# Kernel optimization log

Hardware: AMD Instinct MI355X
Metric: run time of the kernel (lower is better)

The kernel has to match this reference:

```python
import jax, jax.numpy as jnp
import numpy as np

B, N, E = 4, 10000, 80000
DN, DE, DG = 64, 16, 32
D, H, L = 256, 8, 3
DH = D // H


def _ln(x, s, b, eps=1e-6):
    m = x.mean(-1, keepdims=True)
    v = ((x - m) ** 2).mean(-1, keepdims=True)
    return (x - m) * jax.lax.rsqrt(v + eps) * s + b


def setup_inputs() -> dict:
    key = jax.random.key(0)
    ks = jax.random.split(key, 20)
    sc = 0.02
    p = {}
    # graph data
    p['node_features'] = jax.random.normal(ks[0], (B, N, DN), jnp.float32)
    p['edge_features'] = jax.random.normal(ks[1], (B, E, DE), jnp.float32)
    p['global_features'] = jax.random.normal(ks[2], (B, 1, DG), jnp.float32)
    p['edge_list'] = jax.random.randint(ks[3], (B, E, 2), 0, N)
    p['edge_mask'] = jax.random.bernoulli(ks[4], 0.9, (B, E))
    p['node_mask'] = jax.random.bernoulli(ks[5], 0.95, (B, N))
    p['current_agent_node_ind'] = jax.random.randint(ks[6], (B,), 0, N)
    # input projections
    p['W_node_in'] = jax.random.normal(ks[7], (DN + DG, D)) * sc
    p['b_node_in'] = jnp.zeros((D,))
    p['W_edge_in'] = jax.random.normal(ks[8], (DE, D)) * sc
    p['b_edge_in'] = jnp.zeros((D,))
    p['ln_edge_s'] = jnp.ones((D,)); p['ln_edge_b'] = jnp.zeros((D,))
    # stacked GCN layers: message Dense over concat([h_sender, edge_feat])
    p['gcn_W'] = jax.random.normal(ks[9], (L, 2 * D, D)) * sc
    p['gcn_b'] = jnp.zeros((L, D))
    p['ln_s'] = jnp.ones((L, D)); p['ln_b'] = jnp.zeros((L, D))
    # PGAT params
    p['lnq_s'] = jnp.ones((D,)); p['lnq_b'] = jnp.zeros((D,))
    p['lnk_s'] = jnp.ones((D,)); p['lnk_b'] = jnp.zeros((D,))
    p['Wq'] = jax.random.normal(ks[10], (D, D)) * sc; p['bq'] = jnp.zeros((D,))
    p['Wk'] = jax.random.normal(ks[11], (D, D)) * sc; p['bk'] = jnp.zeros((D,))
    p['Wv'] = jax.random.normal(ks[12], (D, D)) * sc; p['bv'] = jnp.zeros((D,))
    p['Wo'] = jax.random.normal(ks[13], (D, D)) * sc; p['bo'] = jnp.zeros((D,))
    p['lnf_s'] = jnp.ones((D,)); p['lnf_b'] = jnp.zeros((D,))
    return p


def reference(node_features, edge_features, global_features, edge_list, edge_mask,
              node_mask, current_agent_node_ind,
              W_node_in, b_node_in, W_edge_in, b_edge_in, ln_edge_s, ln_edge_b,
              gcn_W, gcn_b, ln_s, ln_b,
              lnq_s, lnq_b, lnk_s, lnk_b, Wq, bq, Wk, bk, Wv, bv, Wo, bo,
              lnf_s, lnf_b):
    senders = edge_list[..., 0]
    receivers = edge_list[..., 1]
    # masked-edge handling: original sets indices to -1 so scatter drops them;
    # we mask explicitly (same math) with safe indices.
    s_safe = jnp.where(edge_mask, senders, 0)
    r_safe = jnp.where(edge_mask, receivers, 0)
    emf = edge_mask.astype(node_features.dtype)  # [B, E]

    gf = jnp.broadcast_to(global_features, node_features.shape[:-1] + (DG,))
    h = jnp.concatenate([node_features, gf], axis=-1) @ W_node_in + b_node_in  # [B,N,D]
    e = jax.nn.relu(_ln(edge_features @ W_edge_in + b_edge_in, ln_edge_s, ln_edge_b))  # [B,E,D]

    seg = jax.vmap(lambda m, r: jax.ops.segment_sum(m, r, num_segments=N))
    deg = jnp.maximum(seg(emf[..., None], r_safe), 1.0)  # [B,N,1]

    for i in range(L):
        hn = jax.nn.relu(_ln(h, ln_s[i], ln_b[i]))
        hs = jnp.take_along_axis(hn, s_safe[..., None], axis=-2)  # [B,E,D] gather
        msg = jnp.concatenate([hs, e], axis=-1) @ gcn_W[i] + gcn_b[i]
        msg = msg * emf[..., None]
        agg = seg(msg, r_safe) / deg  # normalized (mean) aggregation
        h = hn + agg  # residual

    # agent node gather: [B,1,D]
    q_in = jnp.take_along_axis(h, current_agent_node_ind[:, None, None], axis=-2)

    # PGAT: masked multi-head attention of agent query over all nodes
    q = _ln(q_in, lnq_s, lnq_b)
    k = _ln(h, lnk_s, lnk_b)
    Q = (q @ Wq + bq).reshape(B, 1, H, DH)
    K = (k @ Wk + bk).reshape(B, N, H, DH)
    V = (k @ Wv + bv).reshape(B, N, H, DH)
    scores = jnp.einsum('bqhd,bkhd->bhqk', Q, K) / jnp.asarray(np.sqrt(DH), Q.dtype)
    scores = jnp.where(node_mask[:, None, None, :], scores, -1e9)
    attn = jax.nn.softmax(scores, axis=-1)
    o = jnp.einsum('bhqk,bkhd->bqhd', attn, V).reshape(B, 1, D)
    x = q_in + (o @ Wo + bo)  # residual
    x = jax.nn.relu(_ln(x, lnf_s, lnf_b))
    return x.reshape(B, D)  # rearrange '... n d -> ... (n d)' with n=1
```

## Files before the change

### kernel.cpp

```cpp
#include <hip/hip_runtime.h>
#include <hip/hip_bf16.h>

#define B_ 4
#define N_ 10000
#define E_ 80000
#define D_ 256
#define BN_ (B_*N_)
#define MPAD 40064
#define SCAN_NBLK ((BN_ + 255) / 256)

typedef __attribute__((ext_vector_type(8))) short short8;
typedef __attribute__((ext_vector_type(4))) float f32x4;
typedef __attribute__((ext_vector_type(4))) unsigned short u16x4;

static __device__ __forceinline__ float wave_sum(float v){
  #pragma unroll
  for(int o=32;o>0;o>>=1) v += __shfl_xor(v, o);
  return v;
}

static __device__ __forceinline__ float block_sum(float v, float* red){
  v = wave_sum(v);
  int w = threadIdx.x >> 6;
  if((threadIdx.x & 63) == 0) red[w] = v;
  __syncthreads();
  float r = (red[0] + red[1]) + (red[2] + red[3]);
  __syncthreads();
  return r;
}

static __device__ __forceinline__ unsigned short f2bf(float f){
  unsigned u = __float_as_uint(f);
  return (unsigned short)((u + 0x7fffu + ((u>>16)&1u)) >> 16);
}
static __device__ __forceinline__ float bf2f(unsigned short b){
  return __uint_as_float(((unsigned)b) << 16);
}

__global__ __launch_bounds__(256) void k_node_in(
    const float* __restrict__ nf, const float* __restrict__ gf,
    const float* __restrict__ W, const float* __restrict__ bias,
    const float* __restrict__ lns, const float* __restrict__ lnb,
    unsigned short* __restrict__ hnbf){
  __shared__ float in_s[16][96];
  __shared__ float h_s[16][256];
  int base = blockIdx.x * 16;
  int tid = threadIdx.x;
  for(int idx = tid; idx < 16*96; idx += 256){
    int i = idx / 96, k = idx - i*96;
    int row = base + i;
    int b = row / N_;
    float v = (k < 64) ? nf[(size_t)row*64 + k] : gf[b*32 + (k-64)];
    in_s[i][k] = v;
  }
  __syncthreads();
  int c = tid;
  float acc[16];
  #pragma unroll
  for(int i=0;i<16;i++) acc[i]=0.f;
  for(int k=0;k<96;k+=4){
    float w0 = W[(k+0)*D_+c], w1 = W[(k+1)*D_+c];
    float w2 = W[(k+2)*D_+c], w3 = W[(k+3)*D_+c];
    #pragma unroll
    for(int i=0;i<16;i++){
      float4 a = *reinterpret_cast<const float4*>(&in_s[i][k]);
      acc[i] += a.x*w0 + a.y*w1 + a.z*w2 + a.w*w3;
    }
  }
  float bc = bias[c];
  #pragma unroll
  for(int i=0;i<16;i++) h_s[i][c] = acc[i] + bc;
  __syncthreads();
  int wv = tid>>6, lane = tid&63;
  float4 s4 = *reinterpret_cast<const float4*>(&lns[lane*4]);
  float4 b4 = *reinterpret_cast<const float4*>(&lnb[lane*4]);
  #pragma unroll
  for(int rr=0; rr<4; ++rr){
    int i = wv*4 + rr;
    float4 x = *reinterpret_cast<const float4*>(&h_s[i][lane*4]);
    float sum = x.x+x.y+x.z+x.w;
    float sq = x.x*x.x+x.y*x.y+x.z*x.z+x.w*x.w;
    #pragma unroll
    for(int o=32;o>0;o>>=1){ sum += __shfl_xor(sum,o); sq += __shfl_xor(sq,o); }
    float mean = sum*(1.f/256.f);
    float var = sq*(1.f/256.f) - mean*mean;
    float rs = rsqrtf(var + 1e-6f);
    u16x4 o;
    o.x = f2bf(fmaxf((x.x-mean)*rs*s4.x + b4.x, 0.f));
    o.y = f2bf(fmaxf((x.y-mean)*rs*s4.y + b4.y, 0.f));
    o.z = f2bf(fmaxf((x.z-mean)*rs*s4.z + b4.z, 0.f));
    o.w = f2bf(fmaxf((x.w-mean)*rs*s4.w + b4.w, 0.f));
    *reinterpret_cast<u16x4*>(&hnbf[(size_t)(base+i)*D_ + lane*4]) = o;
  }
}

__global__ __launch_bounds__(256) void k_hist(
    const int* __restrict__ el, const int* __restrict__ emask,
    int* __restrict__ counts){
  int e = blockIdx.x*256 + threadIdx.x;
  if(e >= B_*E_) return;
  if(emask[e]){
    int b = e / E_;
    int r = el[(size_t)e*2 + 1];
    atomicAdd(&counts[b*N_ + r], 1);
  }
}

__global__ __launch_bounds__(256) void k_scanA(
    const int* __restrict__ counts, int* __restrict__ bsum){
  __shared__ int red[4];
  int idx = blockIdx.x*256 + threadIdx.x;
  int x = (idx < BN_) ? counts[idx] : 0;
  int lane = threadIdx.x & 63, w = threadIdx.x >> 6;
  int s = x;
  #pragma unroll
  for(int o=32;o>0;o>>=1) s += __shfl_xor(s, o);
  if(lane == 0) red[w] = s;
  __syncthreads();
  if(threadIdx.x == 0) bsum[blockIdx.x] = red[0]+red[1]+red[2]+red[3];
}

__global__ __launch_bounds__(256) void k_scanB(
    const int* __restrict__ bsum, int* __restrict__ boff){
  __shared__ int ws[4];
  int t = threadIdx.x;
  int x = (t < SCAN_NBLK) ? bsum[t] : 0;
  int lane = t & 63, w = t >> 6;
  int incl = x;
  #pragma unroll
  for(int o=1;o<64;o<<=1){ int v=__shfl_up(incl,o); if(lane>=o) incl+=v; }
  if(lane == 63) ws[w] = incl;
  __syncthreads();
  int pre = 0;
  for(int i=0;i<w;i++) pre += ws[i];
  if(t < SCAN_NBLK) boff[t] = pre + incl - x;
}

__global__ __launch_bounds__(256) void k_scanC(
    const int* __restrict__ counts, const int* __restrict__ boff,
    int* __restrict__ offsets){
  __shared__ int ws[4];
  int idx = blockIdx.x*256 + threadIdx.x;
  int x = (idx < BN_) ? counts[idx] : 0;
  int lane = threadIdx.x & 63, w = threadIdx.x >> 6;
  int incl = x;
  #pragma unroll
  for(int o=1;o<64;o<<=1){ int v=__shfl_up(incl,o); if(lane>=o) incl+=v; }
  if(lane == 63) ws[w] = incl;
  __syncthreads();
  int pre = boff[blockIdx.x];
  for(int i=0;i<w;i++) pre += ws[i];
  int excl = pre + incl - x;
  if(idx < BN_) offsets[idx] = excl;
  if(idx == BN_-1) offsets[BN_] = excl + x;
}

__global__ __launch_bounds__(256) void k_eprep(
    const float* __restrict__ W, const float* __restrict__ be,
    float* __restrict__ prep){
  int t = threadIdx.x;
  int i = t >> 4, j = t & 15;
  float m = 0.f;
  for(int c=0;c<256;c++) m += W[i*256+c]*W[j*256+c];
  prep[t] = m;
  if(t < 16){
    float v=0.f, wb=0.f;
    for(int c=0;c<256;c++){ v += W[t*256+c]*be[c]; wb += W[t*256+c]; }
    prep[256+t] = v;
    prep[272+t] = wb*(1.f/256.f);
  }
  if(t == 0){
    float bb=0.f, ss=0.f;
    for(int c=0;c<256;c++){ bb += be[c]; ss += be[c]*be[c]; }
    prep[288] = bb*(1.f/256.f);
    prep[289] = ss;
  }
}

__global__ __launch_bounds__(256) void k_fill(
    const int* __restrict__ el, const int* __restrict__ emask,
    const float* __restrict__ ef, const float* __restrict__ prep,
    const int* __restrict__ offsets, int* __restrict__ cursor,
    int* __restrict__ s_send, float* __restrict__ ef_slot,
    float* __restrict__ stats){
  __shared__ float M_s[290];
  for(int i=threadIdx.x; i<290; i+=256) M_s[i] = prep[i];
  __syncthreads();
  int e = blockIdx.x*256 + threadIdx.x;
  if(e >= B_*E_) return;
  if(!emask[e]) return;
  int b = e / E_;
  int s = el[(size_t)e*2], r = el[(size_t)e*2 + 1];
  int bn = b*N_ + r;
  int pos = offsets[bn] + atomicAdd(&cursor[bn], 1);
  s_send[pos] = b*N_ + s;
  const float4* src = reinterpret_cast<const float4*>(ef + (size_t)e*16);
  float4 f0=src[0], f1=src[1], f2=src[2], f3=src[3];
  float4* dst = reinterpret_cast<float4*>(ef_slot + (size_t)pos*16);
  dst[0]=f0; dst[1]=f1; dst[2]=f2; dst[3]=f3;
  float f[16] = {f0.x,f0.y,f0.z,f0.w, f1.x,f1.y,f1.z,f1.w,
                 f2.x,f2.y,f2.z,f2.w, f3.x,f3.y,f3.z,f3.w};
  float mean = M_s[288];
  #pragma unroll
  for(int k=0;k<16;k++) mean += f[k]*M_s[272+k];
  float q = M_s[289];
  #pragma unroll
  for(int i=0;i<16;i++){
    float pi = 2.f*M_s[256+i];
    #pragma unroll
    for(int j=0;j<16;j++) pi += M_s[i*16+j]*f[j];
    q += f[i]*pi;
  }
  float var = q*(1.f/256.f) - mean*mean;
  float rstd = rsqrtf(var + 1e-6f);
  stats[(size_t)pos*2]   = mean;
  stats[(size_t)pos*2+1] = rstd;
}

__global__ __launch_bounds__(256) void k_wt(
    const float* __restrict__ gcnW, unsigned short* __restrict__ Wt){
  __shared__ float sm[32][33];
  int bid = blockIdx.x;
  int l = bid >> 7;
  int t = bid & 127;
  int k0 = (t >> 3)*32, n0 = (t & 7)*32;
  int r = threadIdx.x >> 3;
  int c4 = (threadIdx.x & 7)*4;
  const float* src = gcnW + (size_t)l*512*256;
  float4 v = *reinterpret_cast<const float4*>(&src[(size_t)(k0+r)*256 + n0 + c4]);
  sm[r][c4+0]=v.x; sm[r][c4+1]=v.y; sm[r][c4+2]=v.z; sm[r][c4+3]=v.w;
  __syncthreads();
  u16x4 o;
  o.x = f2bf(sm[c4+0][r]); o.y = f2bf(sm[c4+1][r]);
  o.z = f2bf(sm[c4+2][r]); o.w = f2bf(sm[c4+3][r]);
  *reinterpret_cast<u16x4*>(&Wt[(size_t)l*256*512 + (size_t)(n0+r)*512 + k0 + c4]) = o;
}

#define PROJ(F0,F1,F2,F3,COMP) (be4.COMP \
  + F0.x*w[0].COMP + F0.y*w[1].COMP + F0.z*w[2].COMP + F0.w*w[3].COMP \
  + F1.x*w[4].COMP + F1.y*w[5].COMP + F1.z*w[6].COMP + F1.w*w[7].COMP \
  + F2.x*w[8].COMP + F2.y*w[9].COMP + F2.z*w[10].COMP + F2.w*w[11].COMP \
  + F3.x*w[12].COMP + F3.y*w[13].COMP + F3.z*w[14].COMP + F3.w*w[15].COMP)

__global__ __launch_bounds__(256) void k_se_wave(
    const float* __restrict__ ef_slot, const float* __restrict__ stats,
    const float* __restrict__ W, const float* __restrict__ be,
    const float* __restrict__ lns, const float* __restrict__ lnb,
    const int* __restrict__ offsets, unsigned short* __restrict__ Abf){
  int bn = blockIdx.x*4 + (threadIdx.x>>6);
  int lane = threadIdx.x & 63;
  int c = lane*4;
  float4 w[16];
  #pragma unroll
  for(int k=0;k<16;k++) w[k] = *reinterpret_cast<const float4*>(&W[k*D_ + c]);
  float4 be4 = *reinterpret_cast<const float4*>(&be[c]);
  float4 s4  = *reinterpret_cast<const float4*>(&lns[c]);
  float4 b4  = *reinterpret_cast<const float4*>(&lnb[c]);
  int beg = __builtin_amdgcn_readfirstlane(offsets[bn]);
  int end = __builtin_amdgcn_readfirstlane(offsets[bn+1]);
  float a0=0.f,a1=0.f,a2=0.f,a3=0.f;
  int slot = beg;
  for(; slot+2 <= end; slot += 2){
    const float4* e0 = reinterpret_cast<const float4*>(ef_slot + (size_t)slot*16);
    const float4* e1 = reinterpret_cast<const float4*>(ef_slot + (size_t)(slot+1)*16);
    float2 st0 = *reinterpret_cast<const float2*>(stats + (size_t)slot*2);
    float2 st1 = *reinterpret_cast<const float2*>(stats + (size_t)(slot+1)*2);
    float4 f0=e0[0], f1=e0[1], f2=e0[2], f3=e0[3];
    float4 g0=e1[0], g1=e1[1], g2=e1[2], g3=e1[3];
    float t0=PROJ(f0,f1,f2,f3,x), t1=PROJ(f0,f1,f2,f3,y);
    float t2=PROJ(f0,f1,f2,f3,z), t3=PROJ(f0,f1,f2,f3,w);
    float u0=PROJ(g0,g1,g2,g3,x), u1=PROJ(g0,g1,g2,g3,y);
    float u2=PROJ(g0,g1,g2,g3,z), u3=PROJ(g0,g1,g2,g3,w);
    float m0=st0.x, r0=st0.y, m1=st1.x, r1=st1.y;
    a0 += fmaxf((t0-m0)*r0*s4.x + b4.x, 0.f) + fmaxf((u0-m1)*r1*s4.x + b4.x, 0.f);
    a1 += fmaxf((t1-m0)*r0*s4.y + b4.y, 0.f) + fmaxf((u1-m1)*r1*s4.y + b4.y, 0.f);
    a2 += fmaxf((t2-m0)*r0*s4.z + b4.z, 0.f) + fmaxf((u2-m1)*r1*s4.z + b4.z, 0.f);
    a3 += fmaxf((t3-m0)*r0*s4.w + b4.w, 0.f) + fmaxf((u3-m1)*r1*s4.w + b4.w, 0.f);
  }
  if(slot < end){
    const float4* e0 = reinterpret_cast<const float4*>(ef_slot + (size_t)slot*16);
    float2 st0 = *reinterpret_cast<const float2*>(stats + (size_t)slot*2);
    float4 f0=e0[0], f1=e0[1], f2=e0[2], f3=e0[3];
    float t0=PROJ(f0,f1,f2,f3,x), t1=PROJ(f0,f1,f2,f3,y);
    float t2=PROJ(f0,f1,f2,f3,z), t3=PROJ(f0,f1,f2,f3,w);
    float m0=st0.x, r0=st0.y;
    a0 += fmaxf((t0-m0)*r0*s4.x + b4.x, 0.f);
    a1 += fmaxf((t1-m0)*r0*s4.y + b4.y, 0.f);
    a2 += fmaxf((t2-m0)*r0*s4.z + b4.z, 0.f);
    a3 += fmaxf((t3-m0)*r0*s4.w + b4.w, 0.f);
  }
  u16x4 o; o.x=f2bf(a0); o.y=f2bf(a1); o.z=f2bf(a2); o.w=f2bf(a3);
  *reinterpret_cast<u16x4*>(Abf + (size_t)bn*512 + 256 + c) = o;
}

__global__ __launch_bounds__(256) void k_ln_relu(
    const float* __restrict__ h, const float* __restrict__ s,
    const float* __restrict__ b, unsigned short* __restrict__ hnbf){
  int row = blockIdx.x*4 + (threadIdx.x>>6);
  int lane = threadIdx.x & 63;
  int c = lane*4;
  float4 x = *reinterpret_cast<const float4*>(&h[(size_t)row*D_ + c]);
  float sum = x.x+x.y+x.z+x.w;
  float sq = x.x*x.x+x.y*x.y+x.z*x.z+x.w*x.w;
  #pragma unroll
  for(int o=32;o>0;o>>=1){ sum += __shfl_xor(sum,o); sq += __shfl_xor(sq,o); }
  float mean = sum*(1.f/256.f);
  float var = sq*(1.f/256.f) - mean*mean;
  float rs = rsqrtf(var + 1e-6f);
  float4 s4 = *reinterpret_cast<const float4*>(&s[c]);
  float4 b4 = *reinterpret_cast<const float4*>(&b[c]);
  u16x4 o;
  o.x = f2bf(fmaxf((x.x-mean)*rs*s4.x + b4.x, 0.f));
  o.y = f2bf(fmaxf((x.y-mean)*rs*s4.y + b4.y, 0.f));
  o.z = f2bf(fmaxf((x.z-mean)*rs*s4.z + b4.z, 0.f));
  o.w = f2bf(fmaxf((x.w-mean)*rs*s4.w + b4.w, 0.f));
  *reinterpret_cast<u16x4*>(&hnbf[(size_t)row*D_ + c]) = o;
}

__global__ __launch_bounds__(256) void k_agg(
    const unsigned short* __restrict__ hnbf, const int* __restrict__ offsets,
    const int* __restrict__ s_send, unsigned short* __restrict__ Abf){
  int bn = blockIdx.x*4 + (threadIdx.x>>6);
  int lane = threadIdx.x & 63;
  int beg = __builtin_amdgcn_readfirstlane(offsets[bn]);
  int end = __builtin_amdgcn_readfirstlane(offsets[bn+1]);
  float a0=0.f,a1=0.f,a2=0.f,a3=0.f;
  int slot = beg;
  for(; slot+4 <= end; slot += 4){
    int sr0 = s_send[slot],   sr1 = s_send[slot+1];
    int sr2 = s_send[slot+2], sr3 = s_send[slot+3];
    u16x4 v0 = *reinterpret_cast<const u16x4*>(hnbf + (size_t)sr0*D_ + lane*4);
    u16x4 v1 = *reinterpret_cast<const u16x4*>(hnbf + (size_t)sr1*D_ + lane*4);
    u16x4 v2 = *reinterpret_cast<const u16x4*>(hnbf + (size_t)sr2*D_ + lane*4);
    u16x4 v3 = *reinterpret_cast<const u16x4*>(hnbf + (size_t)sr3*D_ + lane*4);
    a0 += bf2f(v0.x)+bf2f(v1.x)+bf2f(v2.x)+bf2f(v3.x);
    a1 += bf2f(v0.y)+bf2f(v1.y)+bf2f(v2.y)+bf2f(v3.y);
    a2 += bf2f(v0.z)+bf2f(v1.z)+bf2f(v2.z)+bf2f(v3.z);
    a3 += bf2f(v0.w)+bf2f(v1.w)+bf2f(v2.w)+bf2f(v3.w);
  }
  for(; slot < end; ++slot){
    int sr = s_send[slot];
    u16x4 v = *reinterpret_cast<const u16x4*>(hnbf + (size_t)sr*D_ + lane*4);
    a0 += bf2f(v.x); a1 += bf2f(v.y); a2 += bf2f(v.z); a3 += bf2f(v.w);
  }
  u16x4 o; o.x=f2bf(a0); o.y=f2bf(a1); o.z=f2bf(a2); o.w=f2bf(a3);
  *reinterpret_cast<u16x4*>(Abf + (size_t)bn*512 + lane*4) = o;
}

__global__ __launch_bounds__(256) void k_gemm_mfma(
    const unsigned short* __restrict__ Abf,
    const unsigned short* __restrict__ Wt,
    const float* __restrict__ bias,
    const int* __restrict__ counts,
    const unsigned short* __restrict__ hnbf,
    float* __restrict__ hout){
  __shared__ unsigned short A_s[128*32];
  __shared__ unsigned short B_s[128*32];
  int bid = blockIdx.x;
  int row0 = (bid>>1)*128;
  int col0 = (bid&1)*128;
  int tid = threadIdx.x;
  int lane = tid & 63;
  int wid = tid >> 6;
  int wr = wid >> 1, wc = wid & 1;
  f32x4 acc[4][4];
  #pragma unroll
  for(int m=0;m<4;m++)
    #pragma unroll
    for(int n=0;n<4;n++) acc[m][n] = (f32x4){0.f,0.f,0.f,0.f};

  int sr = tid >> 1;
  int sc0 = (tid & 1)*2;
  const unsigned short* agp = Abf + (size_t)(row0+sr)*512;
  const unsigned short* bgp = Wt  + (size_t)(col0+sr)*512;
  unsigned swA0 = (unsigned)(sr*64 + (((sc0  ) ^ (sr&3))*16));
  unsigned swA1 = (unsigned)(sr*64 + (((sc0+1) ^ (sr&3))*16));
  int frow = lane & 15;
  int fsw = (lane >> 4) ^ (lane & 3);

  for(int k0=0; k0<512; k0+=32){
    short8 a0 = *reinterpret_cast<const short8*>(agp + k0 + sc0*8);
    short8 a1 = *reinterpret_cast<const short8*>(agp + k0 + sc0*8 + 8);
    short8 b0 = *reinterpret_cast<const short8*>(bgp + k0 + sc0*8);
    short8 b1 = *reinterpret_cast<const short8*>(bgp + k0 + sc0*8 + 8);
    __syncthreads();
    *reinterpret_cast<short8*>((char*)A_s + swA0) = a0;
    *reinterpret_cast<short8*>((char*)A_s + swA1) = a1;
    *reinterpret_cast<short8*>((char*)B_s + swA0) = b0;
    *reinterpret_cast<short8*>((char*)B_s + swA1) = b1;
    __syncthreads();
    short8 af[4], bfr[4];
    #pragma unroll
    for(int m=0;m<4;m++){
      int r = wr*64 + m*16 + frow;
      af[m] = *reinterpret_cast<const short8*>((const char*)A_s + r*64 + fsw*16);
    }
    #pragma unroll
    for(int n=0;n<4;n++){
      int r = wc*64 + n*16 + frow;
      bfr[n] = *reinterpret_cast<const short8*>((const char*)B_s + r*64 + fsw*16);
    }
    #pragma unroll
    for(int m=0;m<4;m++)
      #pragma unroll
      for(int n=0;n<4;n++)
        acc[m][n] = __builtin_amdgcn_mfma_f32_16x16x32_bf16(af[m], bfr[n], acc[m][n], 0, 0, 0);
  }
  #pragma unroll
  for(int m=0;m<4;m++){
    #pragma unroll
    for(int n=0;n<4;n++){
      int col = col0 + wc*64 + n*16 + (lane&15);
      int rbase = row0 + wr*64 + m*16 + (lane>>4)*4;
      float bcol = bias[col];
      #pragma unroll
      for(int j=0;j<4;j++){
        int r = rbase + j;
        if(r < BN_){
          float cnt = (float)counts[r];
          float inv = 1.f / fmaxf(cnt, 1.f);
          hout[(size_t)r*D_ + col] = bf2f(hnbf[(size_t)r*D_ + col]) + (acc[m][n][j] + cnt*bcol)*inv;
        }
      }
    }
  }
}

__global__ __launch_bounds__(256) void k_qprep(
    const float* __restrict__ h, const int* __restrict__ agent,
    const float* __restrict__ lnq_s, const float* __restrict__ lnq_b,
    const float* __restrict__ Wq, const float* __restrict__ bq,
    const float* __restrict__ Wk, const float* __restrict__ bk,
    float* __restrict__ q_in, float* __restrict__ Wq_eff,
    float* __restrict__ qconst){
  __shared__ float q_s[256];
  __shared__ float Q_s[256];
  __shared__ float red[4];
  int b = blockIdx.x, c = threadIdx.x;
  size_t row = (size_t)(b*N_ + agent[b]);
  float x = h[row*D_ + c];
  q_in[b*D_ + c] = x;
  float s1 = block_sum(x, red);
  float mean = s1*(1.f/256.f);
  float d = x - mean;
  float s2 = block_sum(d*d, red);
  float q = d * rsqrtf(s2*(1.f/256.f) + 1e-6f) * lnq_s[c] + lnq_b[c];
  q_s[c] = q;
  __syncthreads();
  float acc = bq[c];
  for(int k=0;k<256;k++) acc += q_s[k]*Wq[k*D_ + c];
  Q_s[c] = acc;
  __syncthreads();
  const float scale = 0.17677669529663687f;
  for(int idx=c; idx<2048; idx+=256){
    int hh = idx >> 8, dd = idx & 255;
    const float4* wk4 = reinterpret_cast<const float4*>(&Wk[(size_t)dd*D_ + hh*32]);
    const float4* q4  = reinterpret_cast<const float4*>(&Q_s[hh*32]);
    float t = 0.f;
    #pragma unroll
    for(int k4=0;k4<8;k4++){
      float4 w = wk4[k4]; float4 qq = q4[k4];
      t += w.x*qq.x + w.y*qq.y + w.z*qq.z + w.w*qq.w;
    }
    Wq_eff[b*2048 + hh*256 + dd] = t*scale;
  }
  if(c < 8){
    float t = 0.f;
    for(int dh=0; dh<32; dh++) t += Q_s[c*32+dh]*bk[c*32+dh];
    qconst[b*8 + c] = t*scale;
  }
}

__global__ __launch_bounds__(256) void k_scores(
    const float* __restrict__ h, const float* __restrict__ lnk_s,
    const float* __restrict__ lnk_b, const float* __restrict__ Wq_eff,
    const float* __restrict__ qconst, const int* __restrict__ nmask,
    unsigned short* __restrict__ kbuf, float* __restrict__ scores){
  __shared__ float wq_s[2048];
  int row0 = blockIdx.x * 4;
  int b = row0 / N_;
  for(int i=threadIdx.x; i<2048; i+=256) wq_s[i] = Wq_eff[b*2048 + i];
  __syncthreads();
  int wave = threadIdx.x >> 6, lane = threadIdx.x & 63;
  int row = row0 + wave;
  int n = row - b*N_;
  int c = lane*4;
  float4 x = *reinterpret_cast<const float4*>(&h[(size_t)row*D_ + c]);
  float sum = x.x+x.y+x.z+x.w;
  float sq = x.x*x.x+x.y*x.y+x.z*x.z+x.w*x.w;
  #pragma unroll
  for(int o=32;o>0;o>>=1){ sum += __shfl_xor(sum,o); sq += __shfl_xor(sq,o); }
  float mean = sum*(1.f/256.f);
  float var = sq*(1.f/256.f) - mean*mean;
  float rs = rsqrtf(var + 1e-6f);
  float4 s4 = *reinterpret_cast<const float4*>(&lnk_s[c]);
  float4 b4 = *reinterpret_cast<const float4*>(&lnk_b[c]);
  float4 kv;
  kv.x = (x.x-mean)*rs*s4.x + b4.x;
  kv.y = (x.y-mean)*rs*s4.y + b4.y;
  kv.z = (x.z-mean)*rs*s4.z + b4.z;
  kv.w = (x.w-mean)*rs*s4.w + b4.w;
  u16x4 kb; kb.x=f2bf(kv.x); kb.y=f2bf(kv.y); kb.z=f2bf(kv.z); kb.w=f2bf(kv.w);
  *reinterpret_cast<u16x4*>(&kbuf[(size_t)row*D_ + c]) = kb;
  bool valid = nmask[row] != 0;
  #pragma unroll
  for(int hh=0; hh<8; hh++){
    float4 w = *reinterpret_cast<const float4*>(&wq_s[hh*256 + c]);
    float p = kv.x*w.x + kv.y*w.y + kv.z*w.z + kv.w*w.w;
    p = wave_sum(p);
    if(lane==0) scores[(size_t)(b*8+hh)*N_ + n] = valid ? (p + qconst[b*8+hh]) : -1e9f;
  }
}

__global__ __launch_bounds__(256) void k_softA(
    const float* __restrict__ scores, float* __restrict__ pm,
    float* __restrict__ ps){
  __shared__ float red[4];
  int bh = blockIdx.x / 10;
  int c0 = (blockIdx.x % 10) * 1000;
  int tid = threadIdx.x;
  float m = -3e38f;
  for(int n=tid; n<1000; n+=256) m = fmaxf(m, scores[(size_t)bh*N_ + c0 + n]);
  #pragma unroll
  for(int o=32;o>0;o>>=1) m = fmaxf(m, __shfl_xor(m,o));
  if((tid&63)==0) red[tid>>6] = m;
  __syncthreads();
  m = fmaxf(fmaxf(red[0],red[1]), fmaxf(red[2],red[3]));
  __syncthreads();
  float s = 0.f;
  for(int n=tid; n<1000; n+=256) s += __expf(scores[(size_t)bh*N_ + c0 + n] - m);
  s = block_sum(s, red);
  if(tid==0){ pm[blockIdx.x] = m; ps[blockIdx.x] = s; }
}

__global__ __launch_bounds__(64) void k_softB(
    const float* __restrict__ pm, const float* __restrict__ ps,
    float* __restrict__ mg, float* __restrict__ inv){
  int t = threadIdx.x;
  if(t < 32){
    float m = -3e38f;
    #pragma unroll
    for(int c=0;c<10;c++) m = fmaxf(m, pm[t*10+c]);
    float s = 0.f;
    #pragma unroll
    for(int c=0;c<10;c++) s += ps[t*10+c]*__expf(pm[t*10+c]-m);
    mg[t] = m;
    inv[t] = 1.f/s;
  }
}

__global__ __launch_bounds__(256) void k_kbar(
    const unsigned short* __restrict__ kbuf, const float* __restrict__ scores,
    const float* __restrict__ mg, const float* __restrict__ inv,
    float* __restrict__ kbar){
  __shared__ float p_s[8][40];
  int b = blockIdx.x / 250;
  int n0 = (blockIdx.x % 250) * 40;
  for(int i=threadIdx.x; i<8*40; i+=256){
    int hh = i/40, nn = i - hh*40;
    p_s[hh][nn] = __expf(scores[(size_t)(b*8+hh)*N_ + n0 + nn] - mg[b*8+hh]);
  }
  __syncthreads();
  int c = threadIdx.x;
  float acc[8] = {0.f,0.f,0.f,0.f,0.f,0.f,0.f,0.f};
  for(int nn=0; nn<40; ++nn){
    float kv = bf2f(kbuf[(size_t)(b*N_ + n0 + nn)*D_ + c]);
    #pragma unroll
    for(int hh=0;hh<8;hh++) acc[hh] += p_s[hh][nn]*kv;
  }
  #pragma unroll
  for(int hh=0;hh<8;hh++)
    atomicAdd(&kbar[(b*8+hh)*D_ + c], acc[hh]*inv[b*8+hh]);
}

__global__ __launch_bounds__(256) void k_final(
    const float* __restrict__ kbar, const float* __restrict__ Wv,
    const float* __restrict__ bv, const float* __restrict__ Wo,
    const float* __restrict__ bo, const float* __restrict__ q_in,
    const float* __restrict__ lnf_s, const float* __restrict__ lnf_b,
    float* __restrict__ out){
  __shared__ float kb_s[2048];
  __shared__ float o_s[256];
  __shared__ float red[4];
  int b = blockIdx.x, c = threadIdx.x;
  for(int i=c; i<2048; i+=256) kb_s[i] = kbar[b*2048 + i];
  __syncthreads();
  int hh = c >> 5;
  float o = bv[c];
  for(int d=0; d<256; d++) o += kb_s[hh*256 + d]*Wv[(size_t)d*D_ + c];
  o_s[c] = o;
  __syncthreads();
  float y = bo[c] + q_in[b*D_ + c];
  for(int d=0; d<256; d++) y += o_s[d]*Wo[(size_t)d*D_ + c];
  float s1 = block_sum(y, red);
  float mean = s1*(1.f/256.f);
  float dd = y - mean;
  float s2 = block_sum(dd*dd, red);
  float v = dd * rsqrtf(s2*(1.f/256.f) + 1e-6f) * lnf_s[c] + lnf_b[c];
  out[b*D_ + c] = fmaxf(v, 0.f);
}

extern "C" void kernel_launch(void* const* d_in, const int* in_sizes, int n_in,
                              void* d_out, int out_size, void* d_ws, size_t ws_size,
                              hipStream_t stream){
  const float* nf    = (const float*)d_in[0];
  const float* ef    = (const float*)d_in[1];
  const float* gf    = (const float*)d_in[2];
  const int*   el    = (const int*)d_in[3];
  const int*   emask = (const int*)d_in[4];
  const int*   nmask = (const int*)d_in[5];
  const int*   agent = (const int*)d_in[6];
  const float* W_node = (const float*)d_in[7];
  const float* b_node = (const float*)d_in[8];
  const float* W_edge = (const float*)d_in[9];
  const float* b_edge = (const float*)d_in[10];
  const float* ln_e_s = (const float*)d_in[11];
  const float* ln_e_b = (const float*)d_in[12];
  const float* gcn_W  = (const float*)d_in[13];
  const float* gcn_b  = (const float*)d_in[14];
  const float* ln_s   = (const float*)d_in[15];
  const float* ln_b   = (const float*)d_in[16];
  const float* lnq_s  = (const float*)d_in[17];
  const float* lnq_b  = (const float*)d_in[18];
  const float* lnk_s  = (const float*)d_in[19];
  const float* lnk_b  = (const float*)d_in[20];
  const float* Wq = (const float*)d_in[21];
  const float* bq = (const float*)d_in[22];
  const float* Wk = (const float*)d_in[23];
  const float* bk = (const float*)d_in[24];
  const float* Wv = (const float*)d_in[25];
  const float* bv = (const float*)d_in[26];
  const float* Wo = (const float*)d_in[27];
  const float* bo = (const float*)d_in[28];
  const float* lnf_s = (const float*)d_in[29];
  const float* lnf_b = (const float*)d_in[30];
  float* out = (float*)d_out;

  const size_t ND = (size_t)BN_*D_;
  char* w = (char*)d_ws;
  float* h_buf = (float*)w;                   w += ND*4;
  unsigned short* hn_bf = (unsigned short*)w; w += (size_t)MPAD*D_*2;
  unsigned short* A_bf = (unsigned short*)w;  w += (size_t)MPAD*512*2;
  unsigned short* Wt = (unsigned short*)w;    w += (size_t)3*256*512*2;
  float* scores = (float*)w;                  w += (size_t)B_*8*N_*4;
  float* q_in = (float*)w;                    w += B_*D_*4;
  float* Wq_eff = (float*)w;                  w += B_*8*D_*4;
  float* qconst = (float*)w;                  w += B_*8*4;
  float* pm = (float*)w;                      w += 320*4;
  float* ps = (float*)w;                      w += 320*4;
  float* mg = (float*)w;                      w += 32*4;
  float* invs = (float*)w;                    w += 32*4;
  float* kbar = (float*)w;                    w += B_*8*D_*4;
  float* prep = (float*)w;                    w += 512*4;
  int* counts = (int*)w;                      w += BN_*4;
  int* cursor = (int*)w;                      w += BN_*4;
  int* offsets = (int*)w;                     w += (BN_+1)*4;
  int* bsum = (int*)w;                        w += SCAN_NBLK*4;
  int* boff = (int*)w;                        w += SCAN_NBLK*4;
  int* s_send = (int*)w;                      w += (size_t)B_*E_*4;
  float* ef_slot = (float*)w;                 w += (size_t)B_*E_*16*4;
  float* stats = (float*)w;                   w += (size_t)B_*E_*2*4;
  unsigned short* kbuf = (unsigned short*)A_bf;

  hipMemsetAsync(counts, 0, sizeof(int)*(size_t)2*BN_, stream);
  hipMemsetAsync(kbar, 0, sizeof(float)*(size_t)B_*8*D_, stream);

  k_node_in<<<BN_/16, 256, 0, stream>>>(nf, gf, W_node, b_node, ln_s, ln_b, hn_bf);
  k_hist<<<B_*E_/256, 256, 0, stream>>>(el, emask, counts);
  k_scanA<<<SCAN_NBLK, 256, 0, stream>>>(counts, bsum);
  k_scanB<<<1, 256, 0, stream>>>(bsum, boff);
  k_scanC<<<SCAN_NBLK, 256, 0, stream>>>(counts, boff, offsets);
  k_eprep<<<1, 256, 0, stream>>>(W_edge, b_edge, prep);
  k_fill<<<B_*E_/256, 256, 0, stream>>>(el, emask, ef, prep, offsets, cursor,
                                        s_send, ef_slot, stats);
  k_wt<<<384, 256, 0, stream>>>(gcn_W, Wt);
  k_se_wave<<<BN_/4, 256, 0, stream>>>(ef_slot, stats, W_edge, b_edge,
                                       ln_e_s, ln_e_b, offsets, A_bf);

  for(int i=0;i<3;i++){
    k_agg<<<BN_/4, 256, 0, stream>>>(hn_bf, offsets, s_send, A_bf);
    k_gemm_mfma<<<(MPAD/128)*2, 256, 0, stream>>>(A_bf, Wt + (size_t)i*256*512,
                                                  gcn_b + i*D_, counts, hn_bf, h_buf);
    if(i < 2)
      k_ln_relu<<<BN_/4, 256, 0, stream>>>(h_buf, ln_s + (i+1)*D_, ln_b + (i+1)*D_, hn_bf);
  }

  k_qprep<<<B_, 256, 0, stream>>>(h_buf, agent, lnq_s, lnq_b, Wq, bq, Wk, bk,
                                  q_in, Wq_eff, qconst);
  k_scores<<<BN_/4, 256, 0, stream>>>(h_buf, lnk_s, lnk_b, Wq_eff, qconst, nmask,
                                      kbuf, scores);
  k_softA<<<320, 256, 0, stream>>>(scores, pm, ps);
  k_softB<<<1, 64, 0, stream>>>(pm, ps, mg, invs);
  k_kbar<<<B_*250, 256, 0, stream>>>(kbuf, scores, mg, invs, kbar);
  k_final<<<B_, 256, 0, stream>>>(kbar, Wv, bv, Wo, bo, q_in, lnf_s, lnf_b, out);
}
```

Measured before the change: 481.1 us.

## Fuse layer-norm and ReLU into GCN GEMM epilogue with full-row tiles

The GEMM now computes full 256-column rows per block, using 512 threads and a 128x256 tile. This lets the epilogue reduce row statistics through shared memory and apply the next layer's LayerNorm+ReLU directly, writing the bf16 hidden state. The separate ln_relu kernel and the fp32 h round-trip are removed for the first two layers, and ping-pong hn buffers avoid read/write hazards. The cost is halved grid parallelism, more register and LDS pressure, and scattered 2-byte bf16 stores in the epilogue.

```diff
diff --git a/kernel.cpp b/kernel.cpp
--- a/kernel.cpp
+++ b/kernel.cpp
@@ -293,30 +293,6 @@
   *reinterpret_cast<u16x4*>(Abf + (size_t)bn*512 + 256 + c) = o;
 }
 
-__global__ __launch_bounds__(256) void k_ln_relu(
-    const float* __restrict__ h, const float* __restrict__ s,
-    const float* __restrict__ b, unsigned short* __restrict__ hnbf){
-  int row = blockIdx.x*4 + (threadIdx.x>>6);
-  int lane = threadIdx.x & 63;
-  int c = lane*4;
-  float4 x = *reinterpret_cast<const float4*>(&h[(size_t)row*D_ + c]);
-  float sum = x.x+x.y+x.z+x.w;
-  float sq = x.x*x.x+x.y*x.y+x.z*x.z+x.w*x.w;
-  #pragma unroll
-  for(int o=32;o>0;o>>=1){ sum += __shfl_xor(sum,o); sq += __shfl_xor(sq,o); }
-  float mean = sum*(1.f/256.f);
-  float var = sq*(1.f/256.f) - mean*mean;
-  float rs = rsqrtf(var + 1e-6f);
-  float4 s4 = *reinterpret_cast<const float4*>(&s[c]);
-  float4 b4 = *reinterpret_cast<const float4*>(&b[c]);
-  u16x4 o;
-  o.x = f2bf(fmaxf((x.x-mean)*rs*s4.x + b4.x, 0.f));
-  o.y = f2bf(fmaxf((x.y-mean)*rs*s4.y + b4.y, 0.f));
-  o.z = f2bf(fmaxf((x.z-mean)*rs*s4.z + b4.z, 0.f));
-  o.w = f2bf(fmaxf((x.w-mean)*rs*s4.w + b4.w, 0.f));
-  *reinterpret_cast<u16x4*>(&hnbf[(size_t)row*D_ + c]) = o;
-}
-
 __global__ __launch_bounds__(256) void k_agg(
     const unsigned short* __restrict__ hnbf, const int* __restrict__ offsets,
     const int* __restrict__ s_send, unsigned short* __restrict__ Abf){
@@ -347,49 +323,49 @@
   *reinterpret_cast<u16x4*>(Abf + (size_t)bn*512 + lane*4) = o;
 }
 
-__global__ __launch_bounds__(256) void k_gemm_mfma(
+__global__ __launch_bounds__(512) void k_gemm_fused(
     const unsigned short* __restrict__ Abf,
     const unsigned short* __restrict__ Wt,
     const float* __restrict__ bias,
     const int* __restrict__ counts,
-    const unsigned short* __restrict__ hnbf,
-    float* __restrict__ hout){
+    const unsigned short* __restrict__ hn_in,
+    const float* __restrict__ lnsP, const float* __restrict__ lnbP,
+    unsigned short* __restrict__ hn_out,
+    float* __restrict__ h_out){
   __shared__ unsigned short A_s[128*32];
-  __shared__ unsigned short B_s[128*32];
-  int bid = blockIdx.x;
-  int row0 = (bid>>1)*128;
-  int col0 = (bid&1)*128;
+  __shared__ unsigned short B_s[256*32];
+  __shared__ float red_s[2][4][128];
+  int row0 = blockIdx.x * 128;
   int tid = threadIdx.x;
   int lane = tid & 63;
-  int wid = tid >> 6;
-  int wr = wid >> 1, wc = wid & 1;
+  int w = tid >> 6;
+  int wr = w >> 2, wc = w & 3;
+  int q = lane >> 4, frow = lane & 15;
   f32x4 acc[4][4];
   #pragma unroll
   for(int m=0;m<4;m++)
     #pragma unroll
     for(int n=0;n<4;n++) acc[m][n] = (f32x4){0.f,0.f,0.f,0.f};
 
-  int sr = tid >> 1;
-  int sc0 = (tid & 1)*2;
-  const unsigned short* agp = Abf + (size_t)(row0+sr)*512;
-  const unsigned short* bgp = Wt  + (size_t)(col0+sr)*512;
-  unsigned swA0 = (unsigned)(sr*64 + (((sc0  ) ^ (sr&3))*16));
-  unsigned swA1 = (unsigned)(sr*64 + (((sc0+1) ^ (sr&3))*16));
-  int frow = lane & 15;
-  int fsw = (lane >> 4) ^ (lane & 3);
+  int ar = tid >> 2, asc = tid & 3;
+  int br = tid >> 1, bsc0 = (tid & 1)*2;
+  const unsigned short* agp = Abf + (size_t)(row0+ar)*512 + asc*8;
+  const unsigned short* bgp = Wt  + (size_t)br*512 + bsc0*8;
+  unsigned swA  = (unsigned)(ar*64 + ((asc ^ (ar&3))*16));
+  unsigned swB0 = (unsigned)(br*64 + (((bsc0  ) ^ (br&3))*16));
+  unsigned swB1 = (unsigned)(br*64 + (((bsc0+1) ^ (br&3))*16));
+  int fsw = q ^ (lane & 3);
 
   for(int k0=0; k0<512; k0+=32){
-    short8 a0 = *reinterpret_cast<const short8*>(agp + k0 + sc0*8);
-    short8 a1 = *reinterpret_cast<const short8*>(agp + k0 + sc0*8 + 8);
-    short8 b0 = *reinterpret_cast<const short8*>(bgp + k0 + sc0*8);
-    short8 b1 = *reinterpret_cast<const short8*>(bgp + k0 + sc0*8 + 8);
+    short8 av = *reinterpret_cast<const short8*>(agp + k0);
+    short8 b0 = *reinterpret_cast<const short8*>(bgp + k0);
+    short8 b1 = *reinterpret_cast<const short8*>(bgp + k0 + 8);
     __syncthreads();
-    *reinterpret_cast<short8*>((char*)A_s + swA0) = a0;
-    *reinterpret_cast<short8*>((char*)A_s + swA1) = a1;
-    *reinterpret_cast<short8*>((char*)B_s + swA0) = b0;
-    *reinterpret_cast<short8*>((char*)B_s + swA1) = b1;
+    *reinterpret_cast<short8*>((char*)A_s + swA)  = av;
+    *reinterpret_cast<short8*>((char*)B_s + swB0) = b0;
+    *reinterpret_cast<short8*>((char*)B_s + swB1) = b1;
     __syncthreads();
-    short8 af[4], bfr[4];
+    short8 af[4], bf[4];
     #pragma unroll
     for(int m=0;m<4;m++){
       int r = wr*64 + m*16 + frow;
@@ -397,30 +373,78 @@
     }
     #pragma unroll
     for(int n=0;n<4;n++){
-      int r = wc*64 + n*16 + frow;
-      bfr[n] = *reinterpret_cast<const short8*>((const char*)B_s + r*64 + fsw*16);
+      int cc = wc*64 + n*16 + frow;
+      bf[n] = *reinterpret_cast<const short8*>((const char*)B_s + cc*64 + fsw*16);
     }
     #pragma unroll
     for(int m=0;m<4;m++)
       #pragma unroll
       for(int n=0;n<4;n++)
-        acc[m][n] = __builtin_amdgcn_mfma_f32_16x16x32_bf16(af[m], bfr[n], acc[m][n], 0, 0, 0);
-  }
+        acc[m][n] = __builtin_amdgcn_mfma_f32_16x16x32_bf16(af[m], bf[n], acc[m][n], 0, 0, 0);
+  }
+
+  int colbase = wc*64 + frow;
+  float bias4[4];
+  #pragma unroll
+  for(int n=0;n<4;n++) bias4[n] = bias[colbase + n*16];
   #pragma unroll
   for(int m=0;m<4;m++){
     #pragma unroll
-    for(int n=0;n<4;n++){
-      int col = col0 + wc*64 + n*16 + (lane&15);
-      int rbase = row0 + wr*64 + m*16 + (lane>>4)*4;
-      float bcol = bias[col];
+    for(int j=0;j<4;j++){
+      int rl = wr*64 + m*16 + q*4 + j;
+      int row = row0 + rl;
+      float cnt = (row < BN_) ? (float)counts[row] : 1.f;
+      float inv = 1.f / fmaxf(cnt, 1.f);
+      float s = 0.f, s2 = 0.f;
+      #pragma unroll
+      for(int n=0;n<4;n++){
+        int col = colbase + n*16;
+        float hv = (row < BN_) ? bf2f(hn_in[(size_t)row*D_ + col]) : 0.f;
+        float v = hv + (acc[m][n][j] + cnt*bias4[n])*inv;
+        acc[m][n][j] = v;
+        s += v; s2 += v*v;
+      }
+      #pragma unroll
+      for(int o=1;o<16;o<<=1){ s += __shfl_xor(s,o); s2 += __shfl_xor(s2,o); }
+      if(frow == 0){ red_s[0][wc][rl] = s; red_s[1][wc][rl] = s2; }
+    }
+  }
+  __syncthreads();
+  if(lnsP){
+    float lns4[4], lnb4[4];
+    #pragma unroll
+    for(int n=0;n<4;n++){ lns4[n]=lnsP[colbase+n*16]; lnb4[n]=lnbP[colbase+n*16]; }
+    #pragma unroll
+    for(int m=0;m<4;m++){
       #pragma unroll
       for(int j=0;j<4;j++){
-        int r = rbase + j;
-        if(r < BN_){
-          float cnt = (float)counts[r];
-          float inv = 1.f / fmaxf(cnt, 1.f);
-          hout[(size_t)r*D_ + col] = bf2f(hnbf[(size_t)r*D_ + col]) + (acc[m][n][j] + cnt*bcol)*inv;
+        int rl = wr*64 + m*16 + q*4 + j;
+        int row = row0 + rl;
+        if(row >= BN_) continue;
+        float S  = (red_s[0][0][rl]+red_s[0][1][rl]) + (red_s[0][2][rl]+red_s[0][3][rl]);
+        float Q2 = (red_s[1][0][rl]+red_s[1][1][rl]) + (red_s[1][2][rl]+red_s[1][3][rl]);
+        float mean = S*(1.f/256.f);
+        float var = Q2*(1.f/256.f) - mean*mean;
+        float rs = rsqrtf(var + 1e-6f);
+        #pragma unroll
+        for(int n=0;n<4;n++){
+          int col = colbase + n*16;
+          float ov = (acc[m][n][j]-mean)*rs*lns4[n] + lnb4[n];
+          hn_out[(size_t)row*D_ + col] = f2bf(fmaxf(ov, 0.f));
         }
+      }
+    }
+  } else {
+    #pragma unroll
+    for(int m=0;m<4;m++){
+      #pragma unroll
+      for(int j=0;j<4;j++){
+        int rl = wr*64 + m*16 + q*4 + j;
+        int row = row0 + rl;
+        if(row >= BN_) continue;
+        #pragma unroll
+        for(int n=0;n<4;n++)
+          h_out[(size_t)row*D_ + colbase + n*16] = acc[m][n][j];
       }
     }
   }
@@ -639,7 +663,8 @@
   const size_t ND = (size_t)BN_*D_;
   char* w = (char*)d_ws;
   float* h_buf = (float*)w;                   w += ND*4;
-  unsigned short* hn_bf = (unsigned short*)w; w += (size_t)MPAD*D_*2;
+  unsigned short* hnA = (unsigned short*)w;   w += (size_t)MPAD*D_*2;
+  unsigned short* hnB = (unsigned short*)w;   w += (size_t)MPAD*D_*2;
   unsigned short* A_bf = (unsigned short*)w;  w += (size_t)MPAD*512*2;
   unsigned short* Wt = (unsigned short*)w;    w += (size_t)3*256*512*2;
   float* scores = (float*)w;                  w += (size_t)B_*8*N_*4;
@@ -665,7 +690,7 @@
   hipMemsetAsync(counts, 0, sizeof(int)*(size_t)2*BN_, stream);
   hipMemsetAsync(kbar, 0, sizeof(float)*(size_t)B_*8*D_, stream);
 
-  k_node_in<<<BN_/16, 256, 0, stream>>>(nf, gf, W_node, b_node, ln_s, ln_b, hn_bf);
+  k_node_in<<<BN_/16, 256, 0, stream>>>(nf, gf, W_node, b_node, ln_s, ln_b, hnA);
   k_hist<<<B_*E_/256, 256, 0, stream>>>(el, emask, counts);
   k_scanA<<<SCAN_NBLK, 256, 0, stream>>>(counts, bsum);
   k_scanB<<<1, 256, 0, stream>>>(bsum, boff);
@@ -677,12 +702,16 @@
   k_se_wave<<<BN_/4, 256, 0, stream>>>(ef_slot, stats, W_edge, b_edge,
                                        ln_e_s, ln_e_b, offsets, A_bf);
 
+  unsigned short* hin = hnA;
+  unsigned short* hout = hnB;
   for(int i=0;i<3;i++){
-    k_agg<<<BN_/4, 256, 0, stream>>>(hn_bf, offsets, s_send, A_bf);
-    k_gemm_mfma<<<(MPAD/128)*2, 256, 0, stream>>>(A_bf, Wt + (size_t)i*256*512,
-                                                  gcn_b + i*D_, counts, hn_bf, h_buf);
-    if(i < 2)
-      k_ln_relu<<<BN_/4, 256, 0, stream>>>(h_buf, ln_s + (i+1)*D_, ln_b + (i+1)*D_, hn_bf);
+    k_agg<<<BN_/4, 256, 0, stream>>>(hin, offsets, s_send, A_bf);
+    const float* lp = (i<2) ? (ln_s + (i+1)*D_) : nullptr;
+    const float* lb = (i<2) ? (ln_b + (i+1)*D_) : nullptr;
+    k_gemm_fused<<<MPAD/128, 512, 0, stream>>>(A_bf, Wt + (size_t)i*256*512,
+                                               gcn_b + i*D_, counts, hin,
+                                               lp, lb, hout, h_buf);
+    unsigned short* t = hin; hin = hout; hout = t;
   }
 
   k_qprep<<<B_, 256, 0, stream>>>(h_buf, agent, lnq_s, lnq_b, Wq, bq, Wk, bk,
```

After: 534.3 us. +11.0%, slower.
